# Kernel tuning notes

Hardware: AMD Instinct MI355X
Metric: run time of the kernel (lower is better)

Reference implementation:

```python
import jax, jax.numpy as jnp
import numpy as np

B, S, DIM, H, D = 2, 2048, 1024, 16, 64  # inner_dim = H*D = 1024


def setup_inputs() -> dict:
    key = jax.random.key(0)
    ks = jax.random.split(key, 6)
    hidden_states = jax.random.normal(ks[0], (B, S, DIM), dtype=jnp.float32)
    # proper RoPE angle tables for head_dim=D (interleaved-pair convention)
    inv_freq = 1.0 / (10000.0 ** (np.arange(0, D, 2, dtype=np.float32) / D))  # [D/2]
    ang = np.arange(S, dtype=np.float32)[:, None] * inv_freq[None, :]          # [S, D/2]
    ang = np.repeat(ang, 2, axis=-1)                                           # [S, D] interleaved pairs
    cos = jnp.broadcast_to(jnp.asarray(np.cos(ang)), (B, S, D)).astype(jnp.float32)
    sin = jnp.broadcast_to(jnp.asarray(np.sin(ang)), (B, S, D)).astype(jnp.float32)
    scale = 0.02
    qkv_w = jax.random.normal(ks[1], (3 * H * D, DIM), dtype=jnp.float32) * scale
    qkv_b = jax.random.normal(ks[2], (3 * H * D,), dtype=jnp.float32) * scale
    out_w = jax.random.normal(ks[3], (DIM, H * D), dtype=jnp.float32) * scale
    out_b = jax.random.normal(ks[4], (DIM,), dtype=jnp.float32) * scale
    return {"hidden_states": hidden_states, "cos": cos, "sin": sin,
            "qkv_w": qkv_w, "qkv_b": qkv_b, "out_w": out_w, "out_b": out_b}


def _rotate_half_codec(x):
    # interleaved-pair rotation: (x1, x2) -> (-x2, x1) on consecutive pairs
    xr = x.reshape(*x.shape[:-1], -1, 2)
    x1, x2 = xr[..., 0], xr[..., 1]
    return jnp.stack((-x2, x1), axis=-1).reshape(*x.shape)


def reference(hidden_states, cos, sin, qkv_w, qkv_b, out_w, out_b):
    b = hidden_states.shape[0]
    # fused QKV projection: [B,S,DIM] @ [DIM,3*H*D] + bias
    qkv = jnp.einsum('bsd,ed->bse', hidden_states, qkv_w) + qkv_b
    inner = H * D
    q, k, v = qkv[..., :inner], qkv[..., inner:2 * inner], qkv[..., 2 * inner:]
    # [B,S,H*D] -> [B,H,S,D]
    q = q.reshape(b, -1, H, D).transpose(0, 2, 1, 3)
    k = k.reshape(b, -1, H, D).transpose(0, 2, 1, 3)
    v = v.reshape(b, -1, H, D).transpose(0, 2, 1, 3)
    # partial RoPE: applied only to head 0 (query[:, :1], key[:, :1])
    c = cos[:, None]  # [B,1,S,D]
    s = sin[:, None]
    q0 = q[:, :1] * c + _rotate_half_codec(q[:, :1]) * s
    k0 = k[:, :1] * c + _rotate_half_codec(k[:, :1]) * s
    q = jnp.concatenate([q0, q[:, 1:]], axis=1)
    k = jnp.concatenate([k0, k[:, 1:]], axis=1)
    # non-causal SDPA
    scores = jnp.einsum('bhqd,bhkd->bhqk', q, k) / jnp.sqrt(jnp.asarray(D, q.dtype))
    attn = jax.nn.softmax(scores, axis=-1)
    out = jnp.einsum('bhqk,bhkd->bhqd', attn, v)
    out = out.transpose(0, 2, 1, 3).reshape(b, -1, H * D)  # [B,S,H*D]
    # output projection (dropout is identity in eval)
    return jnp.einsum('bse,de->bsd', out, out_w) + out_b
```

## Files before the change

### kernel.cpp

```cpp
#include <hip/hip_runtime.h>
#include <cstdint>

typedef __bf16 bf16x8 __attribute__((ext_vector_type(8)));
typedef float f32x4 __attribute__((ext_vector_type(4)));
typedef float f32x16 __attribute__((ext_vector_type(16)));
typedef unsigned short u16x8 __attribute__((ext_vector_type(8)));
typedef unsigned short u16x4 __attribute__((ext_vector_type(4)));
typedef unsigned int uint32x4 __attribute__((ext_vector_type(4)));
typedef unsigned int uint_g __attribute__((address_space(1)));
typedef unsigned int uint_l __attribute__((address_space(3)));

#define MFMA16(a, b, c) __builtin_amdgcn_mfma_f32_16x16x32_bf16(a, b, c, 0, 0, 0)
#define MFMA32(a, b, c) __builtin_amdgcn_mfma_f32_32x32x16_bf16(a, b, c, 0, 0, 0)

static __device__ __forceinline__ unsigned short f2bf(float f) {
    unsigned u = __builtin_bit_cast(unsigned, f);
    u += 0x7FFFu + ((u >> 16) & 1u);
    return (unsigned short)(u >> 16);
}
static __device__ __forceinline__ float bf2f(unsigned short h) {
    unsigned u = ((unsigned)h) << 16;
    return __builtin_bit_cast(float, u);
}
static __device__ __forceinline__ void gload16(const unsigned short* g, unsigned short* lds) {
    __builtin_amdgcn_global_load_lds((uint_g*)g, (uint_l*)lds, 16, 0, 0);
}
static __device__ __forceinline__ unsigned cvt_pk_bf16(float a, float b) {
    unsigned r;
    asm("v_cvt_pk_bf16_f32 %0, %1, %2" : "=v"(r) : "v"(a), "v"(b));
    return r;
}

#define SB 2048
#define NROWS 4096
#define DIMM 1024
#define NH 16
#define HD 64
#define QSCALE 0.18033688011112043f

__global__ __launch_bounds__(256) void k_convert(const float* __restrict__ s0,
                                                 const float* __restrict__ s1,
                                                 const float* __restrict__ s2,
                                                 unsigned short* __restrict__ dst) {
    int base = blockIdx.x * 256 + threadIdx.x;
#pragma unroll
    for (int v = 0; v < 4; ++v) {
        int i = base + v * 262144;
        const float* src;
        int rel;
        float sc = 1.0f;
        if (i < 524288) { src = s0; rel = i; }
        else if (i < 917504) {
            src = s1; rel = i - 524288;
            if (rel < 131072) sc = QSCALE;
        }
        else { src = s2; rel = i - 917504; }
        const float4* p = (const float4*)src + (size_t)rel * 2;
        float4 a = p[0], bq = p[1];
        u16x8 o;
        o[0] = f2bf(a.x * sc);  o[1] = f2bf(a.y * sc);
        o[2] = f2bf(a.z * sc);  o[3] = f2bf(a.w * sc);
        o[4] = f2bf(bq.x * sc); o[5] = f2bf(bq.y * sc);
        o[6] = f2bf(bq.z * sc); o[7] = f2bf(bq.w * sc);
        *((u16x8*)dst + i) = o;
    }
}

__global__ __launch_bounds__(256) void k_rope(unsigned short* __restrict__ qk,
                                              const float* __restrict__ cosp,
                                              const float* __restrict__ sinp) {
    int gid = blockIdx.x * 256 + threadIdx.x;
    int row = gid >> 4;
    int seg = gid & 15;
    int which = seg >> 3;
    int e0 = (seg & 7) * 8;
    unsigned short* base = qk + (size_t)row * 2048 + which * 1024 + e0;
    u16x8 v = *(u16x8*)base;
    const float* cb = cosp + (size_t)row * 64 + e0;
    const float* sb = sinp + (size_t)row * 64 + e0;
    float4 c0 = *(const float4*)cb, c1 = *(const float4*)(cb + 4);
    float4 s0 = *(const float4*)sb, s1 = *(const float4*)(sb + 4);
    float c[8] = {c0.x, c0.y, c0.z, c0.w, c1.x, c1.y, c1.z, c1.w};
    float s[8] = {s0.x, s0.y, s0.z, s0.w, s1.x, s1.y, s1.z, s1.w};
    u16x8 o;
#pragma unroll
    for (int p = 0; p < 4; ++p) {
        float x0 = bf2f(v[2 * p]);
        float x1 = bf2f(v[2 * p + 1]);
        o[2 * p]     = f2bf(x0 * c[2 * p] - x1 * s[2 * p]);
        o[2 * p + 1] = f2bf(x1 * c[2 * p + 1] + x0 * s[2 * p + 1]);
    }
    *(u16x8*)base = o;
}

template <int MODE, int BM, int NX, int CX, int CY>
__global__ __launch_bounds__(256) void k_gemm_nt(
    const unsigned short* __restrict__ A, const unsigned short* __restrict__ B,
    const float* __restrict__ bias, unsigned short* __restrict__ outQK,
    unsigned short* __restrict__ outVg, float* __restrict__ outF, int M, int N, int K) {
    constexpr int MI = BM / 32;
    __shared__ __align__(16) unsigned short As[BM * 64];
    __shared__ __align__(16) unsigned short Bs[128 * 64];
    const int tid = threadIdx.x;
    const int w = tid >> 6, l = tid & 63, lr = l & 15, lg = l >> 4;
    const int wm = w >> 1, wn = w & 1;

    const int flat = blockIdx.x;
    const int xcd = flat & 7, within = flat >> 3;
    const int bx = (xcd % (NX / CX)) * CX + within % CX;
    const int by = (xcd / (NX / CX)) * CY + within / CX;
    const int m0 = by * BM, n0 = bx * 128;

    f32x4 acc[MI][4];
    f32x4 zero4 = {0.f, 0.f, 0.f, 0.f};
#pragma unroll
    for (int i = 0; i < MI; ++i)
#pragma unroll
        for (int j = 0; j < 4; ++j) acc[i][j] = zero4;

    const int trow = tid >> 3;
    const int tkb = (tid & 7) ^ ((tid >> 3) & 7);
    const unsigned short* Ag = A + (size_t)(m0 + trow) * K + tkb * 8;
    const unsigned short* Bg = B + (size_t)(n0 + trow) * K + tkb * 8;
    const int rsw = (lr & 7) << 3;

    for (int kt = 0; kt < K; kt += 64) {
#pragma unroll
        for (int i = 0; i < BM / 32; ++i)
            gload16(Ag + (size_t)i * 32 * K + kt, (unsigned short*)((char*)As + i * 4096 + w * 1024));
#pragma unroll
        for (int i = 0; i < 4; ++i)
            gload16(Bg + (size_t)i * 32 * K + kt, (unsigned short*)((char*)Bs + i * 4096 + w * 1024));
        asm volatile("s_waitcnt vmcnt(0)" ::: "memory");
        __syncthreads();
        bf16x8 af[MI][2], bfr[4][2];
#pragma unroll
        for (int mi = 0; mi < MI; ++mi)
#pragma unroll
            for (int s = 0; s < 2; ++s)
                af[mi][s] = *(const bf16x8*)&As[(wm * (BM / 2) + mi * 16 + lr) * 64 +
                                                ((s * 32 + lg * 8) ^ rsw)];
#pragma unroll
        for (int ni = 0; ni < 4; ++ni)
#pragma unroll
            for (int s = 0; s < 2; ++s)
                bfr[ni][s] = *(const bf16x8*)&Bs[(wn * 64 + ni * 16 + lr) * 64 +
                                                 ((s * 32 + lg * 8) ^ rsw)];
#pragma unroll
        for (int mi = 0; mi < MI; ++mi)
#pragma unroll
            for (int ni = 0; ni < 4; ++ni)
#pragma unroll
                for (int s = 0; s < 2; ++s)
                    acc[mi][ni] = MFMA16(af[mi][s], bfr[ni][s], acc[mi][ni]);
        __syncthreads();
    }

#pragma unroll
    for (int mi = 0; mi < MI; ++mi)
#pragma unroll
        for (int ni = 0; ni < 4; ++ni) {
            int gc = n0 + wn * 64 + ni * 16 + lr;
            int gr0 = m0 + wm * (BM / 2) + mi * 16 + lg * 4;
            float bv = bias[gc];
            if (MODE == 0 && gc < 1024) bv *= QSCALE;
            f32x4 v = acc[mi][ni];
            if (MODE == 0) {
                if (gc < 2048) {
#pragma unroll
                    for (int r = 0; r < 4; ++r)
                        outQK[(size_t)(gr0 + r) * 2048 + gc] = f2bf(v[r] + bv);
                } else {
                    int e = gc - 2048;
                    int hh = e >> 6, d = e & 63;
                    int bb = gr0 >> 11, s = gr0 & 2047;
                    int bh = bb * NH + hh;
                    int T = s >> 6, w64 = s & 63;
                    int ks = w64 >> 4, hi8 = (w64 >> 3) & 1, j0 = w64 & 7;
                    int db = d >> 5, lqv = d & 31;
                    u16x4 pk;
#pragma unroll
                    for (int r = 0; r < 4; ++r) pk[r] = f2bf(v[r] + bv);
                    size_t off = ((size_t)((bh * 32 + T) * 8 + db * 4 + ks)) * 512 +
                                 (hi8 * 32 + lqv) * 8 + j0;
                    *(u16x4*)&outVg[off] = pk;
                }
            } else {
#pragma unroll
                for (int r = 0; r < 4; ++r)
                    outF[(size_t)(gr0 + r) * N + gc] = v[r] + bv;
            }
        }
}

#define ATTN_BODY(T, PA, VA0, VA1, PB, VB0, VB1, DOSTAGE)                                \
  {                                                                                      \
    if (DOSTAGE) stageK((T) & 1, (T) + 2);                                               \
    const unsigned short* vtbN = vgb + (size_t)((T) + 1) * 4096;                         \
    _Pragma("unroll") for (int ks = 0; ks < 4; ++ks)                                     \
        VB0[ks] = *(const bf16x8*)&vtbN[(size_t)ks * 512 + l * 8];                       \
    _Pragma("unroll") for (int ks = 0; ks < 4; ++ks)                                     \
        VB1[ks] = *(const bf16x8*)&vtbN[(size_t)(4 + ks) * 512 + l * 8];                 \
    const char* Kb = (const char*)Ks[((T) + 1) & 1];                                     \
    f32x16 s0, s1;                                                                       \
    __builtin_amdgcn_s_setprio(1);                                                       \
    _Pragma("unroll") for (int ds = 0; ds < 4; ++ds) {                                   \
        bf16x8 kf0 = *(const bf16x8*)(Kb + lq * 128 + ((ds * 32 + hi * 16) ^ swz));      \
        bf16x8 kf1 = *(const bf16x8*)(Kb + (32 + lq) * 128 + ((ds * 32 + hi * 16) ^ swz)); \
        s0 = (ds == 0) ? MFMA32(kf0, qf[0], z16) : MFMA32(kf0, qf[ds], s0);              \
        s1 = (ds == 0) ? MFMA32(kf1, qf[0], z16) : MFMA32(kf1, qf[ds], s1);              \
    }                                                                                    \
    _Pragma("unroll") for (int ks = 0; ks < 4; ++ks) {                                   \
        oacc[0] = MFMA32(PA[ks], VA0[ks], oacc[0]);                                      \
        oacc[1] = MFMA32(PA[ks], VA1[ks], oacc[1]);                                      \
        lacc    = MFMA32(PA[ks], vones,   lacc);                                         \
    }                                                                                    \
    __builtin_amdgcn_s_setprio(0);                                                       \
    _Pragma("unroll") for (int r = 0; r < 16; ++r) {                                     \
        s0[r] = __builtin_amdgcn_exp2f(s0[r]);                                           \
        s1[r] = __builtin_amdgcn_exp2f(s1[r]);                                           \
    }                                                                                    \
    _Pragma("unroll") for (int ks = 0; ks < 4; ++ks) {                                   \
        const int k2 = ks & 1;                                                           \
        f32x16& sb = (ks < 2) ? s0 : s1;                                                 \
        unsigned XA = cvt_pk_bf16(sb[8 * k2 + 0], sb[8 * k2 + 1]);                       \
        unsigned YA = cvt_pk_bf16(sb[8 * k2 + 2], sb[8 * k2 + 3]);                       \
        unsigned XB = cvt_pk_bf16(sb[8 * k2 + 4], sb[8 * k2 + 5]);                       \
        unsigned YB = cvt_pk_bf16(sb[8 * k2 + 6], sb[8 * k2 + 7]);                       \
        asm("v_permlane32_swap_b32 %0, %1" : "+v"(XA), "+v"(XB));                        \
        asm("v_permlane32_swap_b32 %0, %1" : "+v"(YA), "+v"(YB));                        \
        uint32x4 pw;                                                                     \
        pw[0] = XA; pw[1] = YA; pw[2] = XB; pw[3] = YB;                                  \
        PB[ks] = __builtin_bit_cast(bf16x8, pw);                                         \
    }                                                                                    \
    if (DOSTAGE) {                                                                      \
        asm volatile("s_waitcnt vmcnt(8)" ::: "memory");                                 \
        __builtin_amdgcn_s_barrier();                                                    \
    }                                                                                    \
  }

__global__ __launch_bounds__(128, 2) void k_attn(const unsigned short* __restrict__ qk,
                                                 const unsigned short* __restrict__ vg,
                                                 unsigned short* __restrict__ ao) {
    const int raw = blockIdx.x;
    const int bid = (raw & 7) * 128 + (raw >> 3);
    const int qt = bid & 31, bh = bid >> 5, b = bh >> 4, h = bh & 15;
    const int tid = threadIdx.x, w = tid >> 6, l = tid & 63;
    const int lq = l & 31, hi = l >> 5;

    __shared__ __align__(16) unsigned short Ks[2][4096];

    const size_t rowbase = (size_t)b * SB;
    const int qrow = qt * 64 + w * 32 + lq;

    bf16x8 qf[4];
#pragma unroll
    for (int ds = 0; ds < 4; ++ds)
        qf[ds] = *(const bf16x8*)&qk[(rowbase + qrow) * 2048 + h * 64 + ds * 16 + hi * 8];

    u16x8 onesu;
#pragma unroll
    for (int j = 0; j < 8; ++j) onesu[j] = 0x3F80;
    const bf16x8 vones = __builtin_bit_cast(bf16x8, onesu);

    const char* ksrc[4];
#pragma unroll
    for (int j = 0; j < 4; ++j) {
        int Lb = (j * 2 + w) * 1024 + l * 16;
        int r = Lb >> 7, c = Lb & 127;
        int cs = c ^ ((r & 7) << 4);
        ksrc[j] = (const char*)qk + ((size_t)(rowbase + r) * 2048 + 1024 + h * 64) * 2 + cs;
    }
    auto stageK = [&](int bufi, int tg) {
#pragma unroll
        for (int j = 0; j < 4; ++j)
            gload16((const unsigned short*)(ksrc[j] + (size_t)tg * 262144),
                    Ks[bufi] + (j * 2 + w) * 512);
    };

    const unsigned short* vgb = vg + (size_t)bh * 131072;

    f32x16 z16 = {0.f, 0.f, 0.f, 0.f, 0.f, 0.f, 0.f, 0.f,
                  0.f, 0.f, 0.f, 0.f, 0.f, 0.f, 0.f, 0.f};
    f32x16 oacc[2];
    oacc[0] = z16;
    oacc[1] = z16;
    f32x16 lacc = z16;
    const int swz = (l & 7) << 4;

    bf16x8 vfA0[4], vfA1[4], vfB0[4], vfB1[4];
    bf16x8 paA[4], paB[4];

    stageK(0, 0);
    __syncthreads();
    stageK(1, 1);
#pragma unroll
    for (int ks = 0; ks < 4; ++ks)
        vfA0[ks] = *(const bf16x8*)&vgb[(size_t)ks * 512 + l * 8];
#pragma unroll
    for (int ks = 0; ks < 4; ++ks)
        vfA1[ks] = *(const bf16x8*)&vgb[(size_t)(4 + ks) * 512 + l * 8];
    {
        const char* Kb = (const char*)Ks[0];
        f32x16 s0, s1;
#pragma unroll
        for (int ds = 0; ds < 4; ++ds) {
            bf16x8 kf0 = *(const bf16x8*)(Kb + lq * 128 + ((ds * 32 + hi * 16) ^ swz));
            bf16x8 kf1 = *(const bf16x8*)(Kb + (32 + lq) * 128 + ((ds * 32 + hi * 16) ^ swz));
            s0 = (ds == 0) ? MFMA32(kf0, qf[0], z16) : MFMA32(kf0, qf[ds], s0);
            s1 = (ds == 0) ? MFMA32(kf1, qf[0], z16) : MFMA32(kf1, qf[ds], s1);
        }
#pragma unroll
        for (int r = 0; r < 16; ++r) {
            s0[r] = __builtin_amdgcn_exp2f(s0[r]);
            s1[r] = __builtin_amdgcn_exp2f(s1[r]);
        }
#pragma unroll
        for (int ks = 0; ks < 4; ++ks) {
            const int k2 = ks & 1;
            f32x16& sb = (ks < 2) ? s0 : s1;
            unsigned XA = cvt_pk_bf16(sb[8 * k2 + 0], sb[8 * k2 + 1]);
            unsigned YA = cvt_pk_bf16(sb[8 * k2 + 2], sb[8 * k2 + 3]);
            unsigned XB = cvt_pk_bf16(sb[8 * k2 + 4], sb[8 * k2 + 5]);
            unsigned YB = cvt_pk_bf16(sb[8 * k2 + 6], sb[8 * k2 + 7]);
            asm("v_permlane32_swap_b32 %0, %1" : "+v"(XA), "+v"(XB));
            asm("v_permlane32_swap_b32 %0, %1" : "+v"(YA), "+v"(YB));
            uint32x4 pw;
            pw[0] = XA; pw[1] = YA; pw[2] = XB; pw[3] = YB;
            paA[ks] = __builtin_bit_cast(bf16x8, pw);
        }
    }
    asm volatile("s_waitcnt vmcnt(8)" ::: "memory");
    __builtin_amdgcn_s_barrier();

    for (int tt = 0; tt < 15; ++tt) {
        const int t = 2 * tt;
        ATTN_BODY(t,     paA, vfA0, vfA1, paB, vfB0, vfB1, true)
        ATTN_BODY(t + 1, paB, vfB0, vfB1, paA, vfA0, vfA1, true)
    }
    ATTN_BODY(30, paA, vfA0, vfA1, paB, vfB0, vfB1, false)
    __builtin_amdgcn_s_setprio(1);
#pragma unroll
    for (int ks = 0; ks < 4; ++ks) {
        oacc[0] = MFMA32(paB[ks], vfB0[ks], oacc[0]);
        oacc[1] = MFMA32(paB[ks], vfB1[ks], oacc[1]);
        lacc    = MFMA32(paB[ks], vones,   lacc);
    }
    __builtin_amdgcn_s_setprio(0);

#pragma unroll
    for (int r = 0; r < 16; ++r) {
        float inv = __builtin_amdgcn_rcpf(lacc[r]);
        int qv = (r & 3) + 8 * (r >> 2) + 4 * hi;
        int qg = qt * 64 + w * 32 + qv;
        ao[(rowbase + qg) * DIMM + h * 64 + lq] = f2bf(oacc[0][r] * inv);
        ao[(rowbase + qg) * DIMM + h * 64 + 32 + lq] = f2bf(oacc[1][r] * inv);
    }
}

extern "C" void kernel_launch(void* const* d_in, const int* in_sizes, int n_in,
                              void* d_out, int out_size, void* d_ws, size_t ws_size,
                              hipStream_t stream) {
    const float* hidden = (const float*)d_in[0];
    const float* cosp   = (const float*)d_in[1];
    const float* sinp   = (const float*)d_in[2];
    const float* qkv_w  = (const float*)d_in[3];
    const float* qkv_b  = (const float*)d_in[4];
    const float* out_w  = (const float*)d_in[5];
    const float* out_b  = (const float*)d_in[6];
    float* out = (float*)d_out;

    unsigned short* hbf   = (unsigned short*)d_ws;
    unsigned short* wqkv  = hbf + (size_t)NROWS * DIMM;
    unsigned short* wout  = wqkv + (size_t)3072 * DIMM;
    unsigned short* qkbuf = wout + (size_t)DIMM * DIMM;
    unsigned short* vgbuf = qkbuf + (size_t)NROWS * 2048;
    unsigned short* aobuf = hbf;

    k_convert<<<1024, 256, 0, stream>>>(hidden, qkv_w, out_w, hbf);
    k_gemm_nt<0, 128, 24, 12, 8><<<768, 256, 0, stream>>>(hbf, wqkv, qkv_b, qkbuf, vgbuf,
                                                          nullptr, NROWS, 3072, DIMM);
    k_rope<<<256, 256, 0, stream>>>(qkbuf, cosp, sinp);
    k_attn<<<1024, 128, 0, stream>>>(qkbuf, vgbuf, aobuf);
    k_gemm_nt<1, 64, 8, 8, 8><<<512, 256, 0, stream>>>(aobuf, wout, out_b, nullptr, nullptr,
                                                       out, NROWS, DIMM, DIMM);
}
```

Measured before the change: 112.9 us.

## Double-buffer A tile in LDS and load B fragments directly into registers

Replaces the single-buffered GEMM loop with a two-stage pipeline: the A tile is staged into alternating LDS buffers, while B fragments are read from global memory straight into registers one k-step ahead, ping-ponging between two register sets. MFMA blocks are raised in priority with s_setprio, and the per-iteration vmcnt(0) wait plus two __syncthreads become a partial vmcnt(8) wait and a single barrier. The goal is to overlap global loads with MFMA work and halve the LDS footprint. The loop hardcodes 16 k-steps (K=1024), and the B loads now use uncoalesced per-lane row accesses and more registers.

```diff
diff --git a/kernel.cpp b/kernel.cpp
--- a/kernel.cpp
+++ b/kernel.cpp
@@ -93,14 +93,39 @@
     *(u16x8*)base = o;
 }
 
+#define GEMM_BODY(T, BC, BN, DOSTAGE)                                                    \
+  {                                                                                      \
+    if (DOSTAGE) {                                                                       \
+      stageA(((T) + 1) & 1, ((T) + 1) * 64);                                             \
+      _Pragma("unroll") for (int ni = 0; ni < 4; ++ni)                                   \
+        _Pragma("unroll") for (int s = 0; s < 2; ++s)                                    \
+          BN[ni][s] = *(const bf16x8*)(Bf + (size_t)ni * 16 * K + ((T) + 1) * 64 + s * 32); \
+    }                                                                                    \
+    const unsigned short* Ab = &As[(T) & 1][0];                                          \
+    bf16x8 af[MI][2];                                                                    \
+    _Pragma("unroll") for (int mi = 0; mi < MI; ++mi)                                    \
+      _Pragma("unroll") for (int s = 0; s < 2; ++s)                                      \
+        af[mi][s] = *(const bf16x8*)&Ab[(wm * (BM / 2) + mi * 16 + lr) * 64 +            \
+                                        ((s * 32 + lg * 8) ^ rsw)];                      \
+    __builtin_amdgcn_s_setprio(1);                                                       \
+    _Pragma("unroll") for (int mi = 0; mi < MI; ++mi)                                    \
+      _Pragma("unroll") for (int ni = 0; ni < 4; ++ni)                                   \
+        _Pragma("unroll") for (int s = 0; s < 2; ++s)                                    \
+          acc[mi][ni] = MFMA16(af[mi][s], BC[ni][s], acc[mi][ni]);                       \
+    __builtin_amdgcn_s_setprio(0);                                                       \
+    if (DOSTAGE) {                                                                       \
+      asm volatile("s_waitcnt vmcnt(8)" ::: "memory");                                   \
+      __builtin_amdgcn_s_barrier();                                                      \
+    }                                                                                    \
+  }
+
 template <int MODE, int BM, int NX, int CX, int CY>
 __global__ __launch_bounds__(256) void k_gemm_nt(
     const unsigned short* __restrict__ A, const unsigned short* __restrict__ B,
     const float* __restrict__ bias, unsigned short* __restrict__ outQK,
     unsigned short* __restrict__ outVg, float* __restrict__ outF, int M, int N, int K) {
     constexpr int MI = BM / 32;
-    __shared__ __align__(16) unsigned short As[BM * 64];
-    __shared__ __align__(16) unsigned short Bs[128 * 64];
+    __shared__ __align__(16) unsigned short As[2][BM * 64];
     const int tid = threadIdx.x;
     const int w = tid >> 6, l = tid & 63, lr = l & 15, lg = l >> 4;
     const int wm = w >> 1, wn = w & 1;
@@ -121,40 +146,34 @@
     const int trow = tid >> 3;
     const int tkb = (tid & 7) ^ ((tid >> 3) & 7);
     const unsigned short* Ag = A + (size_t)(m0 + trow) * K + tkb * 8;
-    const unsigned short* Bg = B + (size_t)(n0 + trow) * K + tkb * 8;
     const int rsw = (lr & 7) << 3;
-
-    for (int kt = 0; kt < K; kt += 64) {
+    const unsigned short* Bf = B + (size_t)(n0 + wn * 64 + lr) * K + lg * 8;
+
+    auto stageA = [&](int bufi, int kt) {
 #pragma unroll
         for (int i = 0; i < BM / 32; ++i)
-            gload16(Ag + (size_t)i * 32 * K + kt, (unsigned short*)((char*)As + i * 4096 + w * 1024));
-#pragma unroll
-        for (int i = 0; i < 4; ++i)
-            gload16(Bg + (size_t)i * 32 * K + kt, (unsigned short*)((char*)Bs + i * 4096 + w * 1024));
-        asm volatile("s_waitcnt vmcnt(0)" ::: "memory");
-        __syncthreads();
-        bf16x8 af[MI][2], bfr[4][2];
-#pragma unroll
-        for (int mi = 0; mi < MI; ++mi)
-#pragma unroll
-            for (int s = 0; s < 2; ++s)
-                af[mi][s] = *(const bf16x8*)&As[(wm * (BM / 2) + mi * 16 + lr) * 64 +
-                                                ((s * 32 + lg * 8) ^ rsw)];
-#pragma unroll
-        for (int ni = 0; ni < 4; ++ni)
-#pragma unroll
-            for (int s = 0; s < 2; ++s)
-                bfr[ni][s] = *(const bf16x8*)&Bs[(wn * 64 + ni * 16 + lr) * 64 +
-                                                 ((s * 32 + lg * 8) ^ rsw)];
-#pragma unroll
-        for (int mi = 0; mi < MI; ++mi)
-#pragma unroll
-            for (int ni = 0; ni < 4; ++ni)
-#pragma unroll
-                for (int s = 0; s < 2; ++s)
-                    acc[mi][ni] = MFMA16(af[mi][s], bfr[ni][s], acc[mi][ni]);
-        __syncthreads();
-    }
+            gload16(Ag + (size_t)i * 32 * K + kt,
+                    (unsigned short*)((char*)&As[bufi][0] + i * 4096 + w * 1024));
+    };
+
+    bf16x8 bA[4][2], bB[4][2];
+
+    stageA(0, 0);
+#pragma unroll
+    for (int ni = 0; ni < 4; ++ni)
+#pragma unroll
+        for (int s = 0; s < 2; ++s)
+            bA[ni][s] = *(const bf16x8*)(Bf + (size_t)ni * 16 * K + s * 32);
+    asm volatile("s_waitcnt vmcnt(8)" ::: "memory");
+    __builtin_amdgcn_s_barrier();
+
+    for (int tt = 0; tt < 7; ++tt) {
+        const int t = 2 * tt;
+        GEMM_BODY(t,     bA, bB, true)
+        GEMM_BODY(t + 1, bB, bA, true)
+    }
+    GEMM_BODY(14, bA, bB, true)
+    GEMM_BODY(15, bB, bA, false)
 
 #pragma unroll
     for (int mi = 0; mi < MI; ++mi)
```

Result: slower. 153.0 us (+35.6%).
